# Kernel tuning notes

Hardware: AMD Instinct MI355X
Metric: run time of the kernel (lower is better)

Reference implementation:

```python
import jax, jax.numpy as jnp
import numpy as np

B, S, D = 4, 2048, 1024
H = 16
DH = D // H  # 64
THETA = 10000.0


def setup_inputs() -> dict:
    key = jax.random.key(0)
    ks = jax.random.split(key, 7)
    scale = 1.0 / np.sqrt(D)
    return {
        "Q": jax.random.normal(ks[0], (B, S, D), dtype=jnp.float32),
        "K": jax.random.normal(ks[1], (B, S, D), dtype=jnp.float32),
        "V": jax.random.normal(ks[2], (B, S, D), dtype=jnp.float32),
        "Wq": jax.random.normal(ks[3], (D, D), dtype=jnp.float32) * scale,
        "Wk": jax.random.normal(ks[4], (D, D), dtype=jnp.float32) * scale,
        "Wv": jax.random.normal(ks[5], (D, D), dtype=jnp.float32) * scale,
        "Wo": jax.random.normal(ks[6], (D, D), dtype=jnp.float32) * scale,
    }


def _rope_tables(seq_len, d_head, theta, dtype):
    inv_freq = 1.0 / theta ** (jnp.arange(0, d_head, 2, dtype=jnp.float32) / d_head)
    ang = jnp.arange(seq_len, dtype=jnp.float32)[:, None] * inv_freq[None, :]  # [S, DH/2]
    return jnp.sin(ang).astype(dtype), jnp.cos(ang).astype(dtype)


def _apply_rope(x, sin, cos):
    # x: [B, H, S, DH]; sin/cos: [S, DH/2] broadcast over B,H
    x1 = x[..., 0::2]
    x2 = x[..., 1::2]
    x1r = x1 * cos - x2 * sin
    x2r = x1 * sin + x2 * cos
    return jnp.stack([x1r, x2r], axis=-1).reshape(x.shape)


def reference(Q, K, V, Wq, Wk, Wv, Wo):
    seq_len = Q.shape[-2]
    q = Q @ Wq.T
    k = K @ Wk.T
    v = V @ Wv.T

    def split(x):  # [B, S, D] -> [B, H, S, DH]
        return x.reshape(x.shape[0], seq_len, H, DH).transpose(0, 2, 1, 3)

    qh, kh, vh = split(q), split(k), split(v)

    sin, cos = _rope_tables(seq_len, DH, THETA, qh.dtype)
    qh = _apply_rope(qh, sin, cos)
    kh = _apply_rope(kh, sin, cos)

    # attention in fp32 (matches original cast)
    qf = qh.astype(jnp.float32)
    kf = kh.astype(jnp.float32)
    vf = vh.astype(jnp.float32)
    scale = 1.0 / np.sqrt(DH)
    scores = jnp.einsum('bhqd,bhkd->bhqk', qf, kf) * scale
    causal = jnp.tril(jnp.ones((seq_len, seq_len), dtype=bool))
    scores = jnp.where(causal, scores, -jnp.inf)
    attn = jax.nn.softmax(scores, axis=-1)
    out_h = jnp.einsum('bhqk,bhkd->bhqd', attn, vf).astype(Q.dtype)

    out = out_h.transpose(0, 2, 1, 3).reshape(Q.shape[0], seq_len, D)
    return out @ Wo.T
```

## Files before the change

kernel.cpp:

```cpp
#include <hip/hip_runtime.h>
#include <hip/hip_bf16.h>
#include <cmath>

#define B_ 4
#define S_ 2048
#define D_ 1024
#define H_ 16
#define DH_ 64

typedef __bf16 bf16_t;
typedef __bf16 bf16x8 __attribute__((ext_vector_type(8)));
typedef __bf16 bf16x4 __attribute__((ext_vector_type(4)));
typedef float f32x4 __attribute__((ext_vector_type(4)));

static __device__ __forceinline__ f32x4 mfma16(bf16x8 a, bf16x8 b, f32x4 c) {
    return __builtin_amdgcn_mfma_f32_16x16x32_bf16(a, b, c, 0, 0, 0);
}

static __device__ __forceinline__ float fast_exp2(float x) {
#if __has_builtin(__builtin_amdgcn_exp2f)
    return __builtin_amdgcn_exp2f(x);
#else
    float r; asm("v_exp_f32 %0, %1" : "=v"(r) : "v"(x)); return r;
#endif
}

__global__ void rope_table_kernel(float2* __restrict__ tab) {
    int idx = blockIdx.x * 256 + threadIdx.x;
    int s = idx >> 5, i = idx & 31;
    float inv = powf(10000.f, -(2.f * i) / 64.f);
    float ang = (float)s * inv;
    tab[idx] = make_float2(sinf(ang), cosf(ang));
}

template<int EPI>
__global__ __launch_bounds__(256)
void proj_kernel(const float* __restrict__ X, const float* __restrict__ W,
                 bf16_t* __restrict__ dst, const float2* __restrict__ tab)
{
    __shared__ bf16x8 lA[128 * 8];
    __shared__ bf16x8 lB[128 * 8];
    const int tid = threadIdx.x;
    const int gm0 = blockIdx.x * 128;
    const int gn0 = blockIdx.y * 128;
    const int wid = tid >> 6, lane = tid & 63;
    const int lr = lane & 15, lh = lane >> 4;
    const int wm = (wid >> 1) * 64, wn = (wid & 1) * 64;

    f32x4 acc[4][4] = {};

    for (int kt = 0; kt < D_ / 64; ++kt) {
        const int k0 = kt * 64;
        __syncthreads();
        #pragma unroll
        for (int j = 0; j < 4; ++j) {
            int c = tid + 256 * j;
            int row = c >> 3, sl = c & 7;
            const float* pa = X + (size_t)(gm0 + row) * D_ + k0 + sl * 8;
            float4 a0 = *(const float4*)pa;
            float4 a1 = *(const float4*)(pa + 4);
            bf16x8 va = { (__bf16)a0.x, (__bf16)a0.y, (__bf16)a0.z, (__bf16)a0.w,
                          (__bf16)a1.x, (__bf16)a1.y, (__bf16)a1.z, (__bf16)a1.w };
            lA[row * 8 + (sl ^ (row & 7))] = va;
            const float* pb = W + (size_t)(gn0 + row) * D_ + k0 + sl * 8;
            float4 b0 = *(const float4*)pb;
            float4 b1 = *(const float4*)(pb + 4);
            bf16x8 vb = { (__bf16)b0.x, (__bf16)b0.y, (__bf16)b0.z, (__bf16)b0.w,
                          (__bf16)b1.x, (__bf16)b1.y, (__bf16)b1.z, (__bf16)b1.w };
            lB[row * 8 + (sl ^ (row & 7))] = vb;
        }
        __syncthreads();
        #pragma unroll
        for (int ks = 0; ks < 2; ++ks) {
            bf16x8 af[4], bfr[4];
            int kh = ks * 4 + lh;
            #pragma unroll
            for (int mi = 0; mi < 4; ++mi) { int r = wm + mi * 16 + lr; af[mi]  = lA[r * 8 + (kh ^ (r & 7))]; }
            #pragma unroll
            for (int ni = 0; ni < 4; ++ni) { int r = wn + ni * 16 + lr; bfr[ni] = lB[r * 8 + (kh ^ (r & 7))]; }
            #pragma unroll
            for (int mi = 0; mi < 4; ++mi)
                #pragma unroll
                for (int ni = 0; ni < 4; ++ni)
                    acc[mi][ni] = mfma16(af[mi], bfr[ni], acc[mi][ni]);
        }
    }

    #pragma unroll
    for (int mi = 0; mi < 4; ++mi) {
        #pragma unroll
        for (int j = 0; j < 4; ++j) {
            int m = gm0 + wm + mi * 16 + lh * 4 + j;
            int b = m >> 11, s = m & (S_ - 1);
            #pragma unroll
            for (int ni = 0; ni < 4; ++ni) {
                int n = gn0 + wn + ni * 16 + lr;
                int h = n >> 6, dh = n & 63;
                float x = acc[mi][ni][j];
                if (EPI == 0) {
                    float p = __shfl_xor(x, 1);
                    float2 sc = tab[s * 32 + (dh >> 1)];
                    float r = (dh & 1) ? (p * sc.x + x * sc.y)
                                       : (x * sc.y - p * sc.x);
                    dst[(((size_t)b * H_ + h) * S_ + s) * DH_ + dh] = (bf16_t)r;
                } else {
                    dst[(((size_t)b * H_ + h) * DH_ + dh) * S_ + s] = (bf16_t)x;
                }
            }
        }
    }
}

__global__ __launch_bounds__(512, 4)
void attn_kernel(const bf16_t* __restrict__ qh, const bf16_t* __restrict__ kh,
                 const bf16_t* __restrict__ vT, bf16_t* __restrict__ O)
{
    __shared__ bf16x8 lK[64 * 8];
    __shared__ bf16x8 lV[64 * 8];
    __shared__ bf16x8 lP8[8][128];
    const int tid = threadIdx.x, wid = tid >> 6, lane = tid & 63;
    const int lr = lane & 15, lh = lane >> 4;
    const int bh = blockIdx.x & 63;
    const int p  = blockIdx.x >> 6;
    const bf16_t* Qp = qh + (size_t)bh * S_ * DH_;
    const bf16_t* Kp = kh + (size_t)bh * S_ * DH_;
    const bf16_t* Vp = vT + (size_t)bh * DH_ * S_;
    char* lP = (char*)lP8[wid];
    const int b = bh >> 4, h = bh & 15;
    const float QSCALE = 0.125f * 1.44269504f;

    #pragma unroll 1
    for (int ph = 0; ph < 2; ++ph) {
        const int q0 = (ph == 0 ? (15 - p) : p) * 128;
        const int wq = q0 + wid * 16;

        bf16x8 qf[2];
        #pragma unroll
        for (int ks = 0; ks < 2; ++ks) {
            bf16x8 t = *(const bf16x8*)(Qp + (size_t)(wq + lr) * DH_ + ks * 32 + lh * 8);
            #pragma unroll
            for (int e = 0; e < 8; ++e) t[e] = (__bf16)((float)t[e] * QSCALE);
            qf[ks] = t;
        }

        f32x4 accO[4] = {};
        float mrun = -1e30f, lrun = 0.f;
        const int nkt = q0 / 64 + 2;

        #pragma unroll 1
        for (int kt = 0; kt < nkt; ++kt) {
            __syncthreads();
            {
                int row = tid >> 3, sl = tid & 7;
                lK[row * 8 + (sl ^ (row & 7))] = *(const bf16x8*)(Kp + (size_t)(kt * 64 + row) * DH_ + sl * 8);
                lV[row * 8 + (sl ^ (row & 7))] = *(const bf16x8*)(Vp + (size_t)row * S_ + kt * 64 + sl * 8);
            }
            __syncthreads();

            if (kt * 64 > wq + 15) continue;

            f32x4 sc[4] = {};
            __builtin_amdgcn_s_setprio(1);
            #pragma unroll
            for (int ks = 0; ks < 2; ++ks) {
                int kh8 = ks * 4 + lh;
                #pragma unroll
                for (int kvi = 0; kvi < 4; ++kvi) {
                    int r = kvi * 16 + lr;
                    bf16x8 kf = lK[r * 8 + (kh8 ^ (r & 7))];
                    sc[kvi] = mfma16(kf, qf[ks], sc[kvi]);
                }
            }
            __builtin_amdgcn_s_setprio(0);

            const bool needm = (kt * 64 + 63 > wq);
            const int kvb = kt * 64 + 4 * lh;
            const int qg = wq + lr;
            float pv[16];
            #pragma unroll
            for (int kvi = 0; kvi < 4; ++kvi)
                #pragma unroll
                for (int j = 0; j < 4; ++j) {
                    float x = sc[kvi][j];
                    if (needm && (kvb + kvi * 16 + j) > qg) x = -1e30f;
                    pv[kvi * 4 + j] = x;
                }
            float m8[8], m4v[4];
            #pragma unroll
            for (int i = 0; i < 8; ++i) m8[i] = fmaxf(pv[i], pv[i + 8]);
            #pragma unroll
            for (int i = 0; i < 4; ++i) m4v[i] = fmaxf(m8[i], m8[i + 4]);
            float mx = fmaxf(fmaxf(m4v[0], m4v[2]), fmaxf(m4v[1], m4v[3]));
            mx = fmaxf(mx, __shfl_xor(mx, 16));
            mx = fmaxf(mx, __shfl_xor(mx, 32));

            float mnew;
            float rs = 1.f;
            bool skip = __all(mx <= mrun + 8.0f);
            if (skip) {
                mnew = mrun;
            } else {
                mnew = fmaxf(mrun, mx);
                rs = fast_exp2(mrun - mnew);
                mrun = mnew;
            }
            #pragma unroll
            for (int i = 0; i < 16; ++i) pv[i] = fast_exp2(pv[i] - mnew);
            float s8[8], s4v[4];
            #pragma unroll
            for (int i = 0; i < 8; ++i) s8[i] = pv[i] + pv[i + 8];
            #pragma unroll
            for (int i = 0; i < 4; ++i) s4v[i] = s8[i] + s8[i + 4];
            float sum = (s4v[0] + s4v[1]) + (s4v[2] + s4v[3]);
            sum += __shfl_xor(sum, 16);
            sum += __shfl_xor(sum, 32);

            #pragma unroll
            for (int kvi = 0; kvi < 4; ++kvi) {
                bf16x4 hv = { (__bf16)pv[kvi * 4 + 0], (__bf16)pv[kvi * 4 + 1],
                              (__bf16)pv[kvi * 4 + 2], (__bf16)pv[kvi * 4 + 3] };
                int slot = 2 * kvi + (lh >> 1);
                *(bf16x4*)(lP + lr * 128 + ((slot ^ (lr & 7)) * 16) + (lh & 1) * 8) = hv;
            }

            if (skip) {
                lrun += sum;
            } else {
                lrun = lrun * rs + sum;
                float r = __shfl(rs, 4 * lh + (0));
                #pragma unroll
                for (int j = 0; j < 4; ++j) {
                    float rj = __shfl(rs, 4 * lh + j);
                    #pragma unroll
                    for (int ni = 0; ni < 4; ++ni) accO[ni][j] *= rj;
                }
                (void)r;
            }

            __builtin_amdgcn_s_setprio(1);
            #pragma unroll
            for (int ks = 0; ks < 2; ++ks) {
                int kh8 = ks * 4 + lh;
                int slot = 4 * ks + lh;
                bf16x8 pf = *(const bf16x8*)(lP + lr * 128 + ((slot ^ (lr & 7)) * 16));
                #pragma unroll
                for (int ni = 0; ni < 4; ++ni) {
                    int r = ni * 16 + lr;
                    bf16x8 vf = lV[r * 8 + (kh8 ^ (r & 7))];
                    accO[ni] = mfma16(pf, vf, accO[ni]);
                }
            }
            __builtin_amdgcn_s_setprio(0);
        }

        #pragma unroll
        for (int j = 0; j < 4; ++j) {
            int s = wq + 4 * lh + j;
            float inv = 1.f / __shfl(lrun, 4 * lh + j);
            #pragma unroll
            for (int ni = 0; ni < 4; ++ni) {
                int dh = ni * 16 + lr;
                O[((size_t)(b * S_ + s)) * D_ + h * DH_ + dh] = (bf16_t)(accO[ni][j] * inv);
            }
        }
    }
}

__global__ __launch_bounds__(256)
void out_kernel(const bf16_t* __restrict__ A, const float* __restrict__ W,
                float* __restrict__ out)
{
    __shared__ bf16x8 lA[128 * 8];
    __shared__ bf16x8 lB[128 * 8];
    const int tid = threadIdx.x;
    const int gm0 = blockIdx.x * 128;
    const int gn0 = blockIdx.y * 128;
    const int wid = tid >> 6, lane = tid & 63;
    const int lr = lane & 15, lh = lane >> 4;
    const int wm = (wid >> 1) * 64, wn = (wid & 1) * 64;

    f32x4 acc[4][4] = {};

    for (int kt = 0; kt < D_ / 64; ++kt) {
        const int k0 = kt * 64;
        __syncthreads();
        #pragma unroll
        for (int j = 0; j < 4; ++j) {
            int c = tid + 256 * j;
            int row = c >> 3, sl = c & 7;
            lA[row * 8 + (sl ^ (row & 7))] =
                *(const bf16x8*)(A + (size_t)(gm0 + row) * D_ + k0 + sl * 8);
            const float* pb = W + (size_t)(gn0 + row) * D_ + k0 + sl * 8;
            float4 b0 = *(const float4*)pb;
            float4 b1 = *(const float4*)(pb + 4);
            bf16x8 vb = { (__bf16)b0.x, (__bf16)b0.y, (__bf16)b0.z, (__bf16)b0.w,
                          (__bf16)b1.x, (__bf16)b1.y, (__bf16)b1.z, (__bf16)b1.w };
            lB[row * 8 + (sl ^ (row & 7))] = vb;
        }
        __syncthreads();
        #pragma unroll
        for (int ks = 0; ks < 2; ++ks) {
            bf16x8 af[4], bfr[4];
            int kh = ks * 4 + lh;
            #pragma unroll
            for (int mi = 0; mi < 4; ++mi) { int r = wm + mi * 16 + lr; af[mi]  = lA[r * 8 + (kh ^ (r & 7))]; }
            #pragma unroll
            for (int ni = 0; ni < 4; ++ni) { int r = wn + ni * 16 + lr; bfr[ni] = lB[r * 8 + (kh ^ (r & 7))]; }
            #pragma unroll
            for (int mi = 0; mi < 4; ++mi)
                #pragma unroll
                for (int ni = 0; ni < 4; ++ni)
                    acc[mi][ni] = mfma16(af[mi], bfr[ni], acc[mi][ni]);
        }
    }

    #pragma unroll
    for (int mi = 0; mi < 4; ++mi)
        #pragma unroll
        for (int j = 0; j < 4; ++j) {
            int m = gm0 + wm + mi * 16 + lh * 4 + j;
            #pragma unroll
            for (int ni = 0; ni < 4; ++ni) {
                int n = gn0 + wn + ni * 16 + lr;
                out[(size_t)m * D_ + n] = acc[mi][ni][j];
            }
        }
}

extern "C" void kernel_launch(void* const* d_in, const int* in_sizes, int n_in,
                              void* d_out, int out_size, void* d_ws, size_t ws_size,
                              hipStream_t stream)
{
    const float* Q  = (const float*)d_in[0];
    const float* K  = (const float*)d_in[1];
    const float* V  = (const float*)d_in[2];
    const float* Wq = (const float*)d_in[3];
    const float* Wk = (const float*)d_in[4];
    const float* Wv = (const float*)d_in[5];
    const float* Wo = (const float*)d_in[6];
    float* out = (float*)d_out;

    char* ws = (char*)d_ws;
    const size_t MB = 1024 * 1024;
    bf16_t* qh = (bf16_t*)(ws);
    bf16_t* kh = (bf16_t*)(ws + 16 * MB);
    bf16_t* vT = (bf16_t*)(ws + 32 * MB);
    bf16_t* Ob = (bf16_t*)(ws + 48 * MB);
    float2* tab = (float2*)(ws + 64 * MB);

    rope_table_kernel<<<S_ * 32 / 256, 256, 0, stream>>>(tab);

    dim3 g(64, 8);
    proj_kernel<0><<<g, 256, 0, stream>>>(Q, Wq, qh, tab);
    proj_kernel<0><<<g, 256, 0, stream>>>(K, Wk, kh, tab);
    proj_kernel<1><<<g, 256, 0, stream>>>(V, Wv, vT, tab);

    attn_kernel<<<512, 512, 0, stream>>>(qh, kh, vT, Ob);

    out_kernel<<<g, 256, 0, stream>>>(Ob, Wo, out);
}
```

Measured before the change: 213.6 us.

## Pre-convert inputs and weights to bf16 and load tiles via direct global-to-LDS

Adds separate conversion kernels that turn the fp32 activations and all four weight matrices into bf16 in workspace. The GEMM and attention tile loads then use global_load_lds 16-byte transfers straight into swizzled LDS instead of loading into registers, converting and storing. This removes per-tile conversion work and register staging, and halves the bytes the GEMMs read when tiles are reloaded. In exchange it adds extra passes over the inputs (fp32 read plus bf16 write), more kernel launches, and reuses one workspace buffer for the converted inputs and the attention output.

```diff
diff --git a/kernel.cpp b/kernel.cpp
--- a/kernel.cpp
+++ b/kernel.cpp
@@ -25,6 +25,12 @@
 #endif
 }
 
+static __device__ __forceinline__ void glds16(const bf16_t* g, void* l) {
+    __builtin_amdgcn_global_load_lds(
+        (const __attribute__((address_space(1))) unsigned int*)g,
+        (__attribute__((address_space(3))) unsigned int*)l, 16, 0, 0);
+}
+
 __global__ void rope_table_kernel(float2* __restrict__ tab) {
     int idx = blockIdx.x * 256 + threadIdx.x;
     int s = idx >> 5, i = idx & 31;
@@ -33,9 +39,33 @@
     tab[idx] = make_float2(sinf(ang), cosf(ang));
 }
 
+__global__ __launch_bounds__(256)
+void cvt_kernel(const float* __restrict__ src, bf16_t* __restrict__ dst) {
+    int i = blockIdx.x * 256 + threadIdx.x;
+    const float4* s = (const float4*)(src + (size_t)i * 8);
+    float4 a = s[0], b = s[1];
+    bf16x8 v = { (__bf16)a.x, (__bf16)a.y, (__bf16)a.z, (__bf16)a.w,
+                 (__bf16)b.x, (__bf16)b.y, (__bf16)b.z, (__bf16)b.w };
+    *(bf16x8*)(dst + (size_t)i * 8) = v;
+}
+
+__global__ __launch_bounds__(256)
+void wcvt_kernel(const float* __restrict__ Wq, const float* __restrict__ Wk,
+                 const float* __restrict__ Wv, const float* __restrict__ Wo,
+                 bf16_t* __restrict__ dst) {
+    int i = blockIdx.x * 256 + threadIdx.x;
+    int t = i >> 17, j = i & 131071;
+    const float* src = (t == 0) ? Wq : (t == 1) ? Wk : (t == 2) ? Wv : Wo;
+    const float4* s = (const float4*)(src + (size_t)j * 8);
+    float4 a = s[0], b = s[1];
+    bf16x8 v = { (__bf16)a.x, (__bf16)a.y, (__bf16)a.z, (__bf16)a.w,
+                 (__bf16)b.x, (__bf16)b.y, (__bf16)b.z, (__bf16)b.w };
+    *(bf16x8*)(dst + (size_t)i * 8) = v;
+}
+
 template<int EPI>
 __global__ __launch_bounds__(256)
-void proj_kernel(const float* __restrict__ X, const float* __restrict__ W,
+void proj_kernel(const bf16_t* __restrict__ X, const bf16_t* __restrict__ W,
                  bf16_t* __restrict__ dst, const float2* __restrict__ tab)
 {
     __shared__ bf16x8 lA[128 * 8];
@@ -53,21 +83,12 @@
         const int k0 = kt * 64;
         __syncthreads();
         #pragma unroll
-        for (int j = 0; j < 4; ++j) {
-            int c = tid + 256 * j;
-            int row = c >> 3, sl = c & 7;
-            const float* pa = X + (size_t)(gm0 + row) * D_ + k0 + sl * 8;
-            float4 a0 = *(const float4*)pa;
-            float4 a1 = *(const float4*)(pa + 4);
-            bf16x8 va = { (__bf16)a0.x, (__bf16)a0.y, (__bf16)a0.z, (__bf16)a0.w,
-                          (__bf16)a1.x, (__bf16)a1.y, (__bf16)a1.z, (__bf16)a1.w };
-            lA[row * 8 + (sl ^ (row & 7))] = va;
-            const float* pb = W + (size_t)(gn0 + row) * D_ + k0 + sl * 8;
-            float4 b0 = *(const float4*)pb;
-            float4 b1 = *(const float4*)(pb + 4);
-            bf16x8 vb = { (__bf16)b0.x, (__bf16)b0.y, (__bf16)b0.z, (__bf16)b0.w,
-                          (__bf16)b1.x, (__bf16)b1.y, (__bf16)b1.z, (__bf16)b1.w };
-            lB[row * 8 + (sl ^ (row & 7))] = vb;
+        for (int i = 0; i < 4; ++i) {
+            int base = wid * 64 + i * 256;
+            int slot = base + lane;
+            int row = slot >> 3, s = slot & 7, c = s ^ (row & 7);
+            glds16(X + (size_t)(gm0 + row) * D_ + k0 + c * 8, &lA[base]);
+            glds16(W + (size_t)(gn0 + row) * D_ + k0 + c * 8, &lB[base]);
         }
         __syncthreads();
         #pragma unroll
@@ -151,9 +172,10 @@
         for (int kt = 0; kt < nkt; ++kt) {
             __syncthreads();
             {
-                int row = tid >> 3, sl = tid & 7;
-                lK[row * 8 + (sl ^ (row & 7))] = *(const bf16x8*)(Kp + (size_t)(kt * 64 + row) * DH_ + sl * 8);
-                lV[row * 8 + (sl ^ (row & 7))] = *(const bf16x8*)(Vp + (size_t)row * S_ + kt * 64 + sl * 8);
+                int slot = (wid << 6) + lane;
+                int row = slot >> 3, s = slot & 7, c = s ^ (row & 7);
+                glds16(Kp + (size_t)(kt * 64 + row) * DH_ + c * 8, &lK[wid << 6]);
+                glds16(Vp + (size_t)row * S_ + kt * 64 + c * 8, &lV[wid << 6]);
             }
             __syncthreads();
 
@@ -227,14 +249,12 @@
                 lrun += sum;
             } else {
                 lrun = lrun * rs + sum;
-                float r = __shfl(rs, 4 * lh + (0));
                 #pragma unroll
                 for (int j = 0; j < 4; ++j) {
                     float rj = __shfl(rs, 4 * lh + j);
                     #pragma unroll
                     for (int ni = 0; ni < 4; ++ni) accO[ni][j] *= rj;
                 }
-                (void)r;
             }
 
             __builtin_amdgcn_s_setprio(1);
@@ -267,7 +287,7 @@
 }
 
 __global__ __launch_bounds__(256)
-void out_kernel(const bf16_t* __restrict__ A, const float* __restrict__ W,
+void out_kernel(const bf16_t* __restrict__ A, const bf16_t* __restrict__ W,
                 float* __restrict__ out)
 {
     __shared__ bf16x8 lA[128 * 8];
@@ -285,17 +305,12 @@
         const int k0 = kt * 64;
         __syncthreads();
         #pragma unroll
-        for (int j = 0; j < 4; ++j) {
-            int c = tid + 256 * j;
-            int row = c >> 3, sl = c & 7;
-            lA[row * 8 + (sl ^ (row & 7))] =
-                *(const bf16x8*)(A + (size_t)(gm0 + row) * D_ + k0 + sl * 8);
-            const float* pb = W + (size_t)(gn0 + row) * D_ + k0 + sl * 8;
-            float4 b0 = *(const float4*)pb;
-            float4 b1 = *(const float4*)(pb + 4);
-            bf16x8 vb = { (__bf16)b0.x, (__bf16)b0.y, (__bf16)b0.z, (__bf16)b0.w,
-                          (__bf16)b1.x, (__bf16)b1.y, (__bf16)b1.z, (__bf16)b1.w };
-            lB[row * 8 + (sl ^ (row & 7))] = vb;
+        for (int i = 0; i < 4; ++i) {
+            int base = wid * 64 + i * 256;
+            int slot = base + lane;
+            int row = slot >> 3, s = slot & 7, c = s ^ (row & 7);
+            glds16(A + (size_t)(gm0 + row) * D_ + k0 + c * 8, &lA[base]);
+            glds16(W + (size_t)(gn0 + row) * D_ + k0 + c * 8, &lB[base]);
         }
         __syncthreads();
         #pragma unroll
@@ -342,20 +357,28 @@
 
     char* ws = (char*)d_ws;
     const size_t MB = 1024 * 1024;
-    bf16_t* qh = (bf16_t*)(ws);
-    bf16_t* kh = (bf16_t*)(ws + 16 * MB);
-    bf16_t* vT = (bf16_t*)(ws + 32 * MB);
-    bf16_t* Ob = (bf16_t*)(ws + 48 * MB);
-    float2* tab = (float2*)(ws + 64 * MB);
+    bf16_t* Xbf = (bf16_t*)(ws);
+    bf16_t* Ob  = (bf16_t*)(ws);
+    bf16_t* qh  = (bf16_t*)(ws + 16 * MB);
+    bf16_t* khb = (bf16_t*)(ws + 32 * MB);
+    bf16_t* vT  = (bf16_t*)(ws + 48 * MB);
+    bf16_t* Wb  = (bf16_t*)(ws + 64 * MB);
+    float2* tab = (float2*)(ws + 72 * MB);
 
     rope_table_kernel<<<S_ * 32 / 256, 256, 0, stream>>>(tab);
+    wcvt_kernel<<<2048, 256, 0, stream>>>(Wq, Wk, Wv, Wo, Wb);
 
     dim3 g(64, 8);
-    proj_kernel<0><<<g, 256, 0, stream>>>(Q, Wq, qh, tab);
-    proj_kernel<0><<<g, 256, 0, stream>>>(K, Wk, kh, tab);
-    proj_kernel<1><<<g, 256, 0, stream>>>(V, Wv, vT, tab);
-
-    attn_kernel<<<512, 512, 0, stream>>>(qh, kh, vT, Ob);
-
-    out_kernel<<<g, 256, 0, stream>>>(Ob, Wo, out);
-}
+    const int XBLK = (B_ * S_ * D_) / 8 / 256;
+
+    cvt_kernel<<<XBLK, 256, 0, stream>>>(Q, Xbf);
+    proj_kernel<0><<<g, 256, 0, stream>>>(Xbf, Wb + 0 * 1048576, qh, tab);
+    cvt_kernel<<<XBLK, 256, 0, stream>>>(K, Xbf);
+    proj_kernel<0><<<g, 256, 0, stream>>>(Xbf, Wb + 1 * 1048576, khb, tab);
+    cvt_kernel<<<XBLK, 256, 0, stream>>>(V, Xbf);
+    proj_kernel<1><<<g, 256, 0, stream>>>(Xbf, Wb + 2 * 1048576, vT, tab);
+
+    attn_kernel<<<512, 512, 0, stream>>>(qh, khb, vT, Ob);
+
+    out_kernel<<<g, 256, 0, stream>>>(Ob, Wb + 3 * 1048576, out);
+}
```

Measured after the change: 205.7 us. -3.7%, faster.
